# Performance work log

Hardware: AMD Instinct MI355X
Metric: run time of the kernel (lower is better)

Reference implementation:

```python
import jax, jax.numpy as jnp
import numpy as np

B, H, S, D, R = 2, 32, 1024, 128, 16
NB = 4  # max blocks: pre-image, image, pre-assistant-end, post-assistant


def _make_block_mask():
    # Synthetic but realistic block boundaries per sample (derived from the
    # image-token run and assistant-token subsequence positions that the torch
    # module extracts host-side from input_ids).
    bounds = [
        [(0, 16), (16, 272), (272, 603), (603, S)],
        [(0, 8), (8, 264), (264, 501), (501, S)],
    ]
    m = np.zeros((B, NB, S), np.float32)
    for b, blocks in enumerate(bounds):
        for n, (s, e) in enumerate(blocks):
            m[b, n, s:e] = 1.0
    return jnp.asarray(m)


def setup_inputs() -> dict:
    key = jax.random.key(0)
    ks = jax.random.split(key, 7)
    hid = H * D  # 4096
    lo = H * R   # 512
    causal_masked = ~jnp.tril(jnp.ones((S, S), bool))  # True = masked
    return {
        "query_states": jax.random.normal(ks[0], (B, H, S, D), jnp.float32),
        "key_states": jax.random.normal(ks[1], (B, H, S, D), jnp.float32),
        "Wqa": jax.random.normal(ks[2], (lo, hid), jnp.float32) / np.sqrt(hid),
        "Wqb": jax.random.normal(ks[3], (hid, lo), jnp.float32) / np.sqrt(lo),
        "Wka": jax.random.normal(ks[4], (lo, hid), jnp.float32) / np.sqrt(hid),
        "Wkb": jax.random.normal(ks[5], (hid, lo), jnp.float32) / np.sqrt(lo),
        "alpha": jax.random.normal(ks[6], (1,), jnp.float32) * 0.01,  # alpha_std
        "block_mask": _make_block_mask(),  # [B, NB, K] 1.0 inside block
        "attention_mask": jnp.broadcast_to(causal_masked, (B, 1, S, S)),
    }


def reference(query_states, key_states, Wqa, Wqb, Wka, Wkb, alpha, block_mask, attention_mask):
    Bb, Hh, Q, Dd = query_states.shape
    scaling = Dd ** -0.5

    # low-rank Q projection: [B,H,Q,D] -> [B,Q,H*D] -> rank -> back
    q = query_states.transpose(0, 2, 1, 3).reshape(Bb, Q, Hh * Dd)
    q = (q @ Wqa.T) @ Wqb.T
    q = q.reshape(Bb, Q, Hh, Dd).transpose(0, 2, 1, 3)

    Kk = key_states.shape[2]
    k = key_states.transpose(0, 2, 1, 3).reshape(Bb, Kk, Hh * Dd)
    k = (k @ Wka.T) @ Wkb.T
    k = k.reshape(Bb, Kk, Hh, Dd).transpose(0, 2, 1, 3)

    scores = jnp.einsum('bhqd,bhkd->bhqk', q, k) * scaling  # [B,H,Q,K]
    neg = jnp.finfo(scores.dtype).min
    scores = jnp.where(attention_mask, neg, scores)
    attn = jax.nn.softmax(scores, axis=-1)

    # block-wise mean pooling with causal-valid counts (mean_pool path)
    valid = (~attention_mask[:, 0]).astype(attn.dtype)       # [B,Q,K]
    masked_attn = attn * valid[:, None]                      # zero masked keys
    counts = jnp.einsum('bqk,bnk->bqn', valid, block_mask)   # [B,Q,NB]
    sums = jnp.einsum('bhqk,bnk->bhqn', masked_attn, block_mask)
    block_scores = sums / jnp.maximum(counts, 1.0)[:, None]  # [B,H,Q,NB]

    # expand block scores back to full [B,H,Q,K] and zero masked positions
    reweight = jnp.einsum('bhqn,bnk->bhqk', block_scores, block_mask)
    reweight = reweight * valid[:, None]
    return alpha[0] * reweight
```

## Files before the change

### kernel.cpp

```cpp
#include <hip/hip_runtime.h>
#include <hip/hip_bf16.h>

typedef float    f32x4 __attribute__((ext_vector_type(4)));
typedef _Float16 f16x8 __attribute__((ext_vector_type(8)));
typedef unsigned int u32;

#define S_LEN 1024
#define NHEAD 32
#define DHEAD 128
#define HID   4096
#define LORA  512
#define MROWS 2048

__device__ __forceinline__ void gload16(const void* g, const void* l) {
  __builtin_amdgcn_global_load_lds(
      (const __attribute__((address_space(1))) u32*)g,
      (__attribute__((address_space(3))) u32*)l, 16, 0, 0);
}

#define XCH  1048576
#define WCH  262144
#define TOTCH (2*XCH + 4*WCH)

__global__ __launch_bounds__(256) void convert_kernel(
    const float* __restrict__ Xq, const float* __restrict__ Xk,
    const float* __restrict__ Wqa, const float* __restrict__ Wka,
    const float* __restrict__ Wqb, const float* __restrict__ Wkb,
    _Float16* __restrict__ XqH, _Float16* __restrict__ XkH,
    _Float16* __restrict__ WaqH, _Float16* __restrict__ WakH,
    _Float16* __restrict__ WbqH, _Float16* __restrict__ WbkH)
{
  for (int c = blockIdx.x * 256 + threadIdx.x; c < TOTCH; c += 2048 * 256) {
    const float* src;
    _Float16* dst;
    if (c < 2 * XCH) {
      const int cc = (c < XCH) ? c : c - XCH;
      const float* X = (c < XCH) ? Xq : Xk;
      _Float16*  XH = (c < XCH) ? XqH : XkH;
      const int row = cc >> 9;
      const int col8 = cc & 511;
      const int h = col8 >> 4, d0 = (col8 & 15) * 8;
      const int b = row >> 10, s = row & 1023;
      src = X + (((size_t)(b * NHEAD + h)) * S_LEN + s) * DHEAD + d0;
      dst = XH + (size_t)row * HID + col8 * 8;
    } else {
      const int cw = c - 2 * XCH;
      const int seg = cw / WCH;
      const int off = (cw - seg * WCH) * 8;
      const float* Ws[4] = {Wqa, Wka, Wqb, Wkb};
      _Float16*  Wd[4] = {WaqH, WakH, WbqH, WbkH};
      src = Ws[seg] + off;
      dst = Wd[seg] + off;
    }
    f32x4 v0 = *(const f32x4*)(src + 0);
    f32x4 v1 = *(const f32x4*)(src + 4);
    f16x8 h8;
#pragma unroll
    for (int i = 0; i < 4; ++i) { h8[i] = (_Float16)v0[i]; h8[i + 4] = (_Float16)v1[i]; }
    *(f16x8*)dst = h8;
  }
}

__global__ __launch_bounds__(256) void gemm1_kernel(
    const _Float16* __restrict__ XqH, const _Float16* __restrict__ WaqH,
    const _Float16* __restrict__ XkH, const _Float16* __restrict__ WakH,
    float* __restrict__ Up)
{
  const int side = blockIdx.z >> 2, ks = blockIdx.z & 3;
  const _Float16* A = side ? XkH : XqH;
  const _Float16* B = side ? WakH : WaqH;
  float* U = Up + ((size_t)(side * 4 + ks)) * (MROWS * LORA);

  __shared__ _Float16 As[2][128 * 32];
  __shared__ _Float16 Bs[2][128 * 32];

  const int t = threadIdx.x, lane = t & 63, w = t >> 6;
  const int wr = w >> 1, wc = w & 1;
  const int m0 = blockIdx.x * 128, n0 = blockIdx.y * 128;
  const int kbeg = ks * 1024;

  const int o0 = w * 1024 + lane * 16;
  const int o1 = o0 + 4096;
  const int r0 = o0 >> 6, k0e = (o0 & 63) >> 1;
  const int r1 = o1 >> 6, k1e = (o1 & 63) >> 1;

  f32x4 acc[4][4] = {};

  {
    char* AsB = (char*)As[0]; char* BsB = (char*)Bs[0];
    gload16(A + (size_t)(m0 + r0) * HID + kbeg + k0e, AsB + w * 1024);
    gload16(A + (size_t)(m0 + r1) * HID + kbeg + k1e, AsB + 4096 + w * 1024);
    gload16(B + (size_t)(n0 + r0) * HID + kbeg + k0e, BsB + w * 1024);
    gload16(B + (size_t)(n0 + r1) * HID + kbeg + k1e, BsB + 4096 + w * 1024);
  }
  __syncthreads();

  for (int step = 0; step < 32; ++step) {
    const int cur = step & 1;
    if (step + 1 < 32) {
      const int kt = kbeg + (step + 1) * 32;
      char* AsB = (char*)As[cur ^ 1]; char* BsB = (char*)Bs[cur ^ 1];
      gload16(A + (size_t)(m0 + r0) * HID + kt + k0e, AsB + w * 1024);
      gload16(A + (size_t)(m0 + r1) * HID + kt + k1e, AsB + 4096 + w * 1024);
      gload16(B + (size_t)(n0 + r0) * HID + kt + k0e, BsB + w * 1024);
      gload16(B + (size_t)(n0 + r1) * HID + kt + k1e, BsB + 4096 + w * 1024);
    }
    const char* AsB = (const char*)As[cur];
    const char* BsB = (const char*)Bs[cur];
    f16x8 af[4], bf[4];
#pragma unroll
    for (int im = 0; im < 4; ++im)
      af[im] = *(const f16x8*)(AsB + (wr * 64 + im * 16 + (lane & 15)) * 64 + (lane >> 4) * 16);
#pragma unroll
    for (int in = 0; in < 4; ++in)
      bf[in] = *(const f16x8*)(BsB + (wc * 64 + in * 16 + (lane & 15)) * 64 + (lane >> 4) * 16);
#pragma unroll
    for (int im = 0; im < 4; ++im)
#pragma unroll
      for (int in = 0; in < 4; ++in)
        acc[im][in] = __builtin_amdgcn_mfma_f32_16x16x32_f16(af[im], bf[in], acc[im][in], 0, 0, 0);
    __syncthreads();
  }

#pragma unroll
  for (int im = 0; im < 4; ++im)
#pragma unroll
    for (int in = 0; in < 4; ++in)
#pragma unroll
      for (int j = 0; j < 4; ++j) {
        const int m = m0 + wr * 64 + im * 16 + (lane >> 4) * 4 + j;
        const int n = n0 + wc * 64 + in * 16 + (lane & 15);
        U[(size_t)m * LORA + n] = acc[im][in][j];
      }
}

__global__ __launch_bounds__(256) void reduce_u(
    const float* __restrict__ Up, _Float16* __restrict__ Uq, _Float16* __restrict__ Uk)
{
  const int idx = blockIdx.x * 256 + threadIdx.x;
  const int side = idx >> 17;
  const int cc = idx & 131071;
  const float* base = Up + (size_t)side * 4 * (MROWS * LORA) + (size_t)cc * 8;
  f32x4 s0 = {0.f,0.f,0.f,0.f}, s1 = {0.f,0.f,0.f,0.f};
#pragma unroll
  for (int p = 0; p < 4; ++p) {
    const float* pp = base + (size_t)p * (MROWS * LORA);
    f32x4 a0 = *(const f32x4*)(pp);
    f32x4 a1 = *(const f32x4*)(pp + 4);
    s0 += a0; s1 += a1;
  }
  f16x8 h;
#pragma unroll
  for (int i = 0; i < 4; ++i) { h[i] = (_Float16)s0[i]; h[i + 4] = (_Float16)s1[i]; }
  _Float16* U = side ? Uk : Uq;
  *(f16x8*)(U + (size_t)cc * 8) = h;
}

__global__ __launch_bounds__(256) void gemm2_kernel(
    const _Float16* __restrict__ Uq, const _Float16* __restrict__ WbqH,
    const _Float16* __restrict__ Uk, const _Float16* __restrict__ WbkH,
    _Float16* __restrict__ Pq, _Float16* __restrict__ Pk)
{
  const _Float16* A = blockIdx.z ? Uk : Uq;
  const _Float16* B = blockIdx.z ? WbkH : WbqH;
  _Float16*       P = blockIdx.z ? Pk : Pq;

  __shared__ _Float16 As[2][128 * 32];
  __shared__ _Float16 Bs[2][128 * 32];

  const int t = threadIdx.x, lane = t & 63, w = t >> 6;
  const int wr = w >> 1, wc = w & 1;
  const int m0 = blockIdx.x * 128, n0 = blockIdx.y * 128;

  const int o0 = w * 1024 + lane * 16;
  const int o1 = o0 + 4096;
  const int r0 = o0 >> 6, k0e = (o0 & 63) >> 1;
  const int r1 = o1 >> 6, k1e = (o1 & 63) >> 1;

  f32x4 acc[4][4] = {};

  {
    char* AsB = (char*)As[0]; char* BsB = (char*)Bs[0];
    gload16(A + (size_t)(m0 + r0) * LORA + k0e, AsB + w * 1024);
    gload16(A + (size_t)(m0 + r1) * LORA + k1e, AsB + 4096 + w * 1024);
    gload16(B + (size_t)(n0 + r0) * LORA + k0e, BsB + w * 1024);
    gload16(B + (size_t)(n0 + r1) * LORA + k1e, BsB + 4096 + w * 1024);
  }
  __syncthreads();

  for (int step = 0; step < 16; ++step) {
    const int cur = step & 1;
    if (step + 1 < 16) {
      const int kt = (step + 1) * 32;
      char* AsB = (char*)As[cur ^ 1]; char* BsB = (char*)Bs[cur ^ 1];
      gload16(A + (size_t)(m0 + r0) * LORA + kt + k0e, AsB + w * 1024);
      gload16(A + (size_t)(m0 + r1) * LORA + kt + k1e, AsB + 4096 + w * 1024);
      gload16(B + (size_t)(n0 + r0) * LORA + kt + k0e, BsB + w * 1024);
      gload16(B + (size_t)(n0 + r1) * LORA + kt + k1e, BsB + 4096 + w * 1024);
    }
    const char* AsB = (const char*)As[cur];
    const char* BsB = (const char*)Bs[cur];
    f16x8 af[4], bf[4];
#pragma unroll
    for (int im = 0; im < 4; ++im)
      af[im] = *(const f16x8*)(AsB + (wr * 64 + im * 16 + (lane & 15)) * 64 + (lane >> 4) * 16);
#pragma unroll
    for (int in = 0; in < 4; ++in)
      bf[in] = *(const f16x8*)(BsB + (wc * 64 + in * 16 + (lane & 15)) * 64 + (lane >> 4) * 16);
#pragma unroll
    for (int im = 0; im < 4; ++im)
#pragma unroll
      for (int in = 0; in < 4; ++in)
        acc[im][in] = __builtin_amdgcn_mfma_f32_16x16x32_f16(af[im], bf[in], acc[im][in], 0, 0, 0);
    __syncthreads();
  }

#pragma unroll
  for (int im = 0; im < 4; ++im)
#pragma unroll
    for (int in = 0; in < 4; ++in)
#pragma unroll
      for (int j = 0; j < 4; ++j) {
        const int m = m0 + wr * 64 + im * 16 + (lane >> 4) * 4 + j;
        const int n = n0 + wc * 64 + in * 16 + (lane & 15);
        P[(size_t)m * HID + n] = (_Float16)acc[im][in][j];
      }
}

__global__ __launch_bounds__(256) void attn_kernel(
    const _Float16* __restrict__ QP, const _Float16* __restrict__ KP,
    const float* __restrict__ bmask, const float* __restrict__ alphap,
    float* __restrict__ out)
{
  __shared__ float    bm[1024 * 4];
  __shared__ float    pf[1024 * 4];
  __shared__ _Float16 kv[64 * 136];
  __shared__ float    bs_l[64 * 4];

  const int t = threadIdx.x;
  const int lane = t & 63, w = t >> 6;
  const int bh = blockIdx.x, b = bh >> 5, h = bh & 31;
  const int qb = (int)(gridDim.y - 1) - (int)blockIdx.y;

  for (int idx = t; idx < 4096; idx += 256) {
    const int nb = idx >> 10, k = idx & 1023;
    bm[k * 4 + nb] = bmask[(size_t)b * 4096 + idx];
  }
  __syncthreads();

  {
    float carry = 0.f;
    for (int seg = 0; seg < 16; ++seg) {
      float v = bm[(seg * 64 + lane) * 4 + w];
#pragma unroll
      for (int d = 1; d < 64; d <<= 1) {
        float u = __shfl_up(v, d, 64);
        if (lane >= d) v += u;
      }
      pf[(seg * 64 + lane) * 4 + w] = v + carry;
      carry += __shfl(v, 63, 64);
    }
  }

  const int qrow = qb * 64 + w * 16 + (lane & 15);
  const _Float16* qrp = QP + (size_t)(b * 1024 + qrow) * HID + h * DHEAD;
  f16x8 a[4];
#pragma unroll
  for (int i = 0; i < 4; ++i)
    a[i] = *(const f16x8*)(qrp + i * 32 + (lane >> 4) * 8);

  float bsum[4][4] = {};
  const float scale = 0.08838834764831845f;

  const int r = t >> 2, c = (t & 3) * 32;
  const _Float16* kbase = KP + (size_t)(b * 1024) * HID + h * DHEAD;

  for (int kt = 0; kt <= qb; ++kt) {
    const _Float16* pk = kbase + (size_t)(kt * 64 + r) * HID + c;
    f16x8 k0 = *(const f16x8*)(pk + 0);
    f16x8 k1 = *(const f16x8*)(pk + 8);
    f16x8 k2 = *(const f16x8*)(pk + 16);
    f16x8 k3 = *(const f16x8*)(pk + 24);
    __syncthreads();
    *(f16x8*)&kv[r * 136 + c + 0]  = k0;
    *(f16x8*)&kv[r * 136 + c + 8]  = k1;
    *(f16x8*)&kv[r * 136 + c + 16] = k2;
    *(f16x8*)&kv[r * 136 + c + 24] = k3;
    __syncthreads();

    const bool last = (kt == qb);
#pragma unroll
    for (int nt = 0; nt < 4; ++nt) {
      if (last && nt > w) break;
      f32x4 sacc = {0.f, 0.f, 0.f, 0.f};
#pragma unroll
      for (int i = 0; i < 4; ++i) {
        f16x8 bf = *(const f16x8*)&kv[(nt * 16 + (lane & 15)) * 136 + i * 32 + (lane >> 4) * 8];
        sacc = __builtin_amdgcn_mfma_f32_16x16x32_f16(a[i], bf, sacc, 0, 0, 0);
      }
      const int kk = kt * 64 + nt * 16 + (lane & 15);
      f32x4 mv = *(const f32x4*)&bm[kk * 4];
      const bool diag = last && (nt == w);
#pragma unroll
      for (int j = 0; j < 4; ++j) {
        float e = __expf(sacc[j] * scale);
        if (diag) {
          const int q = qb * 64 + w * 16 + (lane >> 4) * 4 + j;
          e = (kk <= q) ? e : 0.f;
        }
        bsum[0][j] += e * mv[0];
        bsum[1][j] += e * mv[1];
        bsum[2][j] += e * mv[2];
        bsum[3][j] += e * mv[3];
      }
    }
  }

#pragma unroll
  for (int j = 0; j < 4; ++j)
#pragma unroll
    for (int m = 1; m < 16; m <<= 1)
#pragma unroll
      for (int nb = 0; nb < 4; ++nb)
        bsum[nb][j] += __shfl_xor(bsum[nb][j], m, 64);

  const float alpha = alphap[0];
  if ((lane & 15) == 0) {
#pragma unroll
    for (int j = 0; j < 4; ++j) {
      const int rr = w * 16 + (lane >> 4) * 4 + j;
      const int q = qb * 64 + rr;
      const float Lr = bsum[0][j] + bsum[1][j] + bsum[2][j] + bsum[3][j];
      const float ainvL = alpha / Lr;
#pragma unroll
      for (int nb = 0; nb < 4; ++nb)
        bs_l[rr * 4 + nb] = bsum[nb][j] * ainvL / fmaxf(pf[q * 4 + nb], 1.f);
    }
  }
  __syncthreads();

  const size_t obase = ((size_t)bh * 1024 + (size_t)qb * 64) * 1024;
  const int k0 = t * 4;
  f32x4 m0v = *(const f32x4*)&bm[(k0 + 0) * 4];
  f32x4 m1v = *(const f32x4*)&bm[(k0 + 1) * 4];
  f32x4 m2v = *(const f32x4*)&bm[(k0 + 2) * 4];
  f32x4 m3v = *(const f32x4*)&bm[(k0 + 3) * 4];
  for (int rr = 0; rr < 64; ++rr) {
    const int q = qb * 64 + rr;
    f32x4 bsv = *(const f32x4*)&bs_l[rr * 4];
    f32x4 o;
    o[0] = (k0 + 0 <= q) ? (bsv[0]*m0v[0] + bsv[1]*m0v[1] + bsv[2]*m0v[2] + bsv[3]*m0v[3]) : 0.f;
    o[1] = (k0 + 1 <= q) ? (bsv[0]*m1v[0] + bsv[1]*m1v[1] + bsv[2]*m1v[2] + bsv[3]*m1v[3]) : 0.f;
    o[2] = (k0 + 2 <= q) ? (bsv[0]*m2v[0] + bsv[1]*m2v[1] + bsv[2]*m2v[2] + bsv[3]*m2v[3]) : 0.f;
    o[3] = (k0 + 3 <= q) ? (bsv[0]*m3v[0] + bsv[1]*m3v[1] + bsv[2]*m3v[2] + bsv[3]*m3v[3]) : 0.f;
    *(f32x4*)(out + obase + (size_t)rr * 1024 + k0) = o;
  }
}

extern "C" void kernel_launch(void* const* d_in, const int* in_sizes, int n_in,
                              void* d_out, int out_size, void* d_ws, size_t ws_size,
                              hipStream_t stream) {
  const float* q     = (const float*)d_in[0];
  const float* k     = (const float*)d_in[1];
  const float* Wqa   = (const float*)d_in[2];
  const float* Wqb   = (const float*)d_in[3];
  const float* Wka   = (const float*)d_in[4];
  const float* Wkb   = (const float*)d_in[5];
  const float* alpha = (const float*)d_in[6];
  const float* bmask = (const float*)d_in[7];
  float* out = (float*)d_out;

  _Float16* XqH  = (_Float16*)d_ws;
  _Float16* XkH  = XqH  + (size_t)MROWS * HID;
  _Float16* WaqH = XkH  + (size_t)MROWS * HID;
  _Float16* WakH = WaqH + (size_t)LORA * HID;
  _Float16* WbqH = WakH + (size_t)LORA * HID;
  _Float16* WbkH = WbqH + (size_t)HID * LORA;
  _Float16* Uq   = WbkH + (size_t)HID * LORA;
  _Float16* Uk   = Uq   + (size_t)MROWS * LORA;
  _Float16* Pq   = Uk   + (size_t)MROWS * LORA;
  _Float16* Pk   = Pq   + (size_t)MROWS * HID;
  float*    Up   = (float*)(Pk + (size_t)MROWS * HID);

  convert_kernel<<<2048, 256, 0, stream>>>(q, k, Wqa, Wka, Wqb, Wkb,
                                           XqH, XkH, WaqH, WakH, WbqH, WbkH);
  gemm1_kernel<<<dim3(16, 4, 8), 256, 0, stream>>>(XqH, WaqH, XkH, WakH, Up);
  reduce_u    <<<1024, 256, 0, stream>>>(Up, Uq, Uk);
  gemm2_kernel<<<dim3(16, 32, 2), 256, 0, stream>>>(Uq, WbqH, Uk, WbkH, Pq, Pk);
  attn_kernel <<<dim3(64, 16), 256, 0, stream>>>(Pq, Pk, bmask, alpha, out);
}
```

Baseline: 457.8 us.

## Fuse fp32-to-fp16 conversion into GEMM loads and prefetch K tiles in attention

```diff
diff --git a/kernel.cpp b/kernel.cpp
--- a/kernel.cpp
+++ b/kernel.cpp
@@ -18,57 +18,23 @@
       (__attribute__((address_space(3))) u32*)l, 16, 0, 0);
 }
 
-#define XCH  1048576
-#define WCH  262144
-#define TOTCH (2*XCH + 4*WCH)
-
-__global__ __launch_bounds__(256) void convert_kernel(
-    const float* __restrict__ Xq, const float* __restrict__ Xk,
-    const float* __restrict__ Wqa, const float* __restrict__ Wka,
-    const float* __restrict__ Wqb, const float* __restrict__ Wkb,
-    _Float16* __restrict__ XqH, _Float16* __restrict__ XkH,
-    _Float16* __restrict__ WaqH, _Float16* __restrict__ WakH,
-    _Float16* __restrict__ WbqH, _Float16* __restrict__ WbkH)
-{
-  for (int c = blockIdx.x * 256 + threadIdx.x; c < TOTCH; c += 2048 * 256) {
-    const float* src;
-    _Float16* dst;
-    if (c < 2 * XCH) {
-      const int cc = (c < XCH) ? c : c - XCH;
-      const float* X = (c < XCH) ? Xq : Xk;
-      _Float16*  XH = (c < XCH) ? XqH : XkH;
-      const int row = cc >> 9;
-      const int col8 = cc & 511;
-      const int h = col8 >> 4, d0 = (col8 & 15) * 8;
-      const int b = row >> 10, s = row & 1023;
-      src = X + (((size_t)(b * NHEAD + h)) * S_LEN + s) * DHEAD + d0;
-      dst = XH + (size_t)row * HID + col8 * 8;
-    } else {
-      const int cw = c - 2 * XCH;
-      const int seg = cw / WCH;
-      const int off = (cw - seg * WCH) * 8;
-      const float* Ws[4] = {Wqa, Wka, Wqb, Wkb};
-      _Float16*  Wd[4] = {WaqH, WakH, WbqH, WbkH};
-      src = Ws[seg] + off;
-      dst = Wd[seg] + off;
-    }
-    f32x4 v0 = *(const f32x4*)(src + 0);
-    f32x4 v1 = *(const f32x4*)(src + 4);
-    f16x8 h8;
-#pragma unroll
-    for (int i = 0; i < 4; ++i) { h8[i] = (_Float16)v0[i]; h8[i + 4] = (_Float16)v1[i]; }
-    *(f16x8*)dst = h8;
-  }
+__device__ __forceinline__ f16x8 cvt8(f32x4 a, f32x4 b) {
+  f16x8 r;
+  r[0] = (_Float16)a[0]; r[1] = (_Float16)a[1];
+  r[2] = (_Float16)a[2]; r[3] = (_Float16)a[3];
+  r[4] = (_Float16)b[0]; r[5] = (_Float16)b[1];
+  r[6] = (_Float16)b[2]; r[7] = (_Float16)b[3];
+  return r;
 }
 
 __global__ __launch_bounds__(256) void gemm1_kernel(
-    const _Float16* __restrict__ XqH, const _Float16* __restrict__ WaqH,
-    const _Float16* __restrict__ XkH, const _Float16* __restrict__ WakH,
+    const float* __restrict__ Xq, const float* __restrict__ Wqa_,
+    const float* __restrict__ Xk, const float* __restrict__ Wka_,
     float* __restrict__ Up)
 {
   const int side = blockIdx.z >> 2, ks = blockIdx.z & 3;
-  const _Float16* A = side ? XkH : XqH;
-  const _Float16* B = side ? WakH : WaqH;
+  const float* X = side ? Xk : Xq;
+  const float* W = side ? Wka_ : Wqa_;
   float* U = Up + ((size_t)(side * 4 + ks)) * (MROWS * LORA);
 
   __shared__ _Float16 As[2][128 * 32];
@@ -79,47 +45,47 @@
   const int m0 = blockIdx.x * 128, n0 = blockIdx.y * 128;
   const int kbeg = ks * 1024;
 
-  const int o0 = w * 1024 + lane * 16;
-  const int o1 = o0 + 4096;
-  const int r0 = o0 >> 6, k0e = (o0 & 63) >> 1;
-  const int r1 = o1 >> 6, k1e = (o1 & 63) >> 1;
-
+  const int ar = t >> 1, ac = (t & 1) * 16;
+  const int am = m0 + ar, ab = am >> 10, as_ = am & 1023;
+  const float* Abase = X + (size_t)ab * (NHEAD * S_LEN * DHEAD) + (size_t)as_ * DHEAD;
+  const float* Brow = W + (size_t)(n0 + ar) * HID;
+
+  f16x8 ha0, ha1, hb0, hb1;
+  auto LOADREGS = [&](int kt) {
+    const int kg = kt + ac;
+    const float* pa = Abase + (size_t)(kg >> 7) * (S_LEN * DHEAD) + (kg & 127);
+    f32x4 a0 = *(const f32x4*)(pa + 0), a1 = *(const f32x4*)(pa + 4);
+    f32x4 a2 = *(const f32x4*)(pa + 8), a3 = *(const f32x4*)(pa + 12);
+    const float* pb = Brow + kg;
+    f32x4 b0 = *(const f32x4*)(pb + 0), b1 = *(const f32x4*)(pb + 4);
+    f32x4 b2 = *(const f32x4*)(pb + 8), b3 = *(const f32x4*)(pb + 12);
+    ha0 = cvt8(a0, a1); ha1 = cvt8(a2, a3);
+    hb0 = cvt8(b0, b1); hb1 = cvt8(b2, b3);
+  };
+
+  LOADREGS(kbeg);
   f32x4 acc[4][4] = {};
-
-  {
-    char* AsB = (char*)As[0]; char* BsB = (char*)Bs[0];
-    gload16(A + (size_t)(m0 + r0) * HID + kbeg + k0e, AsB + w * 1024);
-    gload16(A + (size_t)(m0 + r1) * HID + kbeg + k1e, AsB + 4096 + w * 1024);
-    gload16(B + (size_t)(n0 + r0) * HID + kbeg + k0e, BsB + w * 1024);
-    gload16(B + (size_t)(n0 + r1) * HID + kbeg + k1e, BsB + 4096 + w * 1024);
-  }
-  __syncthreads();
 
   for (int step = 0; step < 32; ++step) {
     const int cur = step & 1;
-    if (step + 1 < 32) {
-      const int kt = kbeg + (step + 1) * 32;
-      char* AsB = (char*)As[cur ^ 1]; char* BsB = (char*)Bs[cur ^ 1];
-      gload16(A + (size_t)(m0 + r0) * HID + kt + k0e, AsB + w * 1024);
-      gload16(A + (size_t)(m0 + r1) * HID + kt + k1e, AsB + 4096 + w * 1024);
-      gload16(B + (size_t)(n0 + r0) * HID + kt + k0e, BsB + w * 1024);
-      gload16(B + (size_t)(n0 + r1) * HID + kt + k1e, BsB + 4096 + w * 1024);
-    }
-    const char* AsB = (const char*)As[cur];
-    const char* BsB = (const char*)Bs[cur];
+    *(f16x8*)&As[cur][ar * 32 + ac]     = ha0;
+    *(f16x8*)&As[cur][ar * 32 + ac + 8] = ha1;
+    *(f16x8*)&Bs[cur][ar * 32 + ac]     = hb0;
+    *(f16x8*)&Bs[cur][ar * 32 + ac + 8] = hb1;
+    __syncthreads();
+    if (step + 1 < 32) LOADREGS(kbeg + (step + 1) * 32);
     f16x8 af[4], bf[4];
 #pragma unroll
     for (int im = 0; im < 4; ++im)
-      af[im] = *(const f16x8*)(AsB + (wr * 64 + im * 16 + (lane & 15)) * 64 + (lane >> 4) * 16);
+      af[im] = *(const f16x8*)&As[cur][(wr * 64 + im * 16 + (lane & 15)) * 32 + (lane >> 4) * 8];
 #pragma unroll
     for (int in = 0; in < 4; ++in)
-      bf[in] = *(const f16x8*)(BsB + (wc * 64 + in * 16 + (lane & 15)) * 64 + (lane >> 4) * 16);
+      bf[in] = *(const f16x8*)&Bs[cur][(wc * 64 + in * 16 + (lane & 15)) * 32 + (lane >> 4) * 8];
 #pragma unroll
     for (int im = 0; im < 4; ++im)
 #pragma unroll
       for (int in = 0; in < 4; ++in)
         acc[im][in] = __builtin_amdgcn_mfma_f32_16x16x32_f16(af[im], bf[in], acc[im][in], 0, 0, 0);
-    __syncthreads();
   }
 
 #pragma unroll
@@ -145,9 +111,8 @@
 #pragma unroll
   for (int p = 0; p < 4; ++p) {
     const float* pp = base + (size_t)p * (MROWS * LORA);
-    f32x4 a0 = *(const f32x4*)(pp);
-    f32x4 a1 = *(const f32x4*)(pp + 4);
-    s0 += a0; s1 += a1;
+    s0 += *(const f32x4*)(pp);
+    s1 += *(const f32x4*)(pp + 4);
   }
   f16x8 h;
 #pragma unroll
@@ -157,12 +122,12 @@
 }
 
 __global__ __launch_bounds__(256) void gemm2_kernel(
-    const _Float16* __restrict__ Uq, const _Float16* __restrict__ WbqH,
-    const _Float16* __restrict__ Uk, const _Float16* __restrict__ WbkH,
+    const _Float16* __restrict__ Uq, const float* __restrict__ Wqb_,
+    const _Float16* __restrict__ Uk, const float* __restrict__ Wkb_,
     _Float16* __restrict__ Pq, _Float16* __restrict__ Pk)
 {
   const _Float16* A = blockIdx.z ? Uk : Uq;
-  const _Float16* B = blockIdx.z ? WbkH : WbqH;
+  const float*   Wf = blockIdx.z ? Wkb_ : Wqb_;
   _Float16*       P = blockIdx.z ? Pk : Pq;
 
   __shared__ _Float16 As[2][128 * 32];
@@ -177,42 +142,44 @@
   const int r0 = o0 >> 6, k0e = (o0 & 63) >> 1;
   const int r1 = o1 >> 6, k1e = (o1 & 63) >> 1;
 
+  const int ar = t >> 1, ac = (t & 1) * 16;
+  const float* Brow = Wf + (size_t)(n0 + ar) * LORA;
+
+  auto GLOADA = [&](int buf, int kt) {
+    char* AsB = (char*)As[buf];
+    gload16(A + (size_t)(m0 + r0) * LORA + kt + k0e, AsB + w * 1024);
+    gload16(A + (size_t)(m0 + r1) * LORA + kt + k1e, AsB + 4096 + w * 1024);
+  };
+  f16x8 hb0, hb1;
+  auto LOADB = [&](int kt) {
+    const float* pb = Brow + kt + ac;
+    f32x4 b0 = *(const f32x4*)(pb + 0), b1 = *(const f32x4*)(pb + 4);
+    f32x4 b2 = *(const f32x4*)(pb + 8), b3 = *(const f32x4*)(pb + 12);
+    hb0 = cvt8(b0, b1); hb1 = cvt8(b2, b3);
+  };
+
+  LOADB(0);
+  GLOADA(0, 0);
   f32x4 acc[4][4] = {};
-
-  {
-    char* AsB = (char*)As[0]; char* BsB = (char*)Bs[0];
-    gload16(A + (size_t)(m0 + r0) * LORA + k0e, AsB + w * 1024);
-    gload16(A + (size_t)(m0 + r1) * LORA + k1e, AsB + 4096 + w * 1024);
-    gload16(B + (size_t)(n0 + r0) * LORA + k0e, BsB + w * 1024);
-    gload16(B + (size_t)(n0 + r1) * LORA + k1e, BsB + 4096 + w * 1024);
-  }
-  __syncthreads();
 
   for (int step = 0; step < 16; ++step) {
     const int cur = step & 1;
-    if (step + 1 < 16) {
-      const int kt = (step + 1) * 32;
-      char* AsB = (char*)As[cur ^ 1]; char* BsB = (char*)Bs[cur ^ 1];
-      gload16(A + (size_t)(m0 + r0) * LORA + kt + k0e, AsB + w * 1024);
-      gload16(A + (size_t)(m0 + r1) * LORA + kt + k1e, AsB + 4096 + w * 1024);
-      gload16(B + (size_t)(n0 + r0) * LORA + kt + k0e, BsB + w * 1024);
-      gload16(B + (size_t)(n0 + r1) * LORA + kt + k1e, BsB + 4096 + w * 1024);
-    }
-    const char* AsB = (const char*)As[cur];
-    const char* BsB = (const char*)Bs[cur];
+    *(f16x8*)&Bs[cur][ar * 32 + ac]     = hb0;
+    *(f16x8*)&Bs[cur][ar * 32 + ac + 8] = hb1;
+    __syncthreads();
+    if (step + 1 < 16) { LOADB((step + 1) * 32); GLOADA(cur ^ 1, (step + 1) * 32); }
     f16x8 af[4], bf[4];
 #pragma unroll
     for (int im = 0; im < 4; ++im)
-      af[im] = *(const f16x8*)(AsB + (wr * 64 + im * 16 + (lane & 15)) * 64 + (lane >> 4) * 16);
+      af[im] = *(const f16x8*)&As[cur][(wr * 64 + im * 16 + (lane & 15)) * 32 + (lane >> 4) * 8];
 #pragma unroll
     for (int in = 0; in < 4; ++in)
-      bf[in] = *(const f16x8*)(BsB + (wc * 64 + in * 16 + (lane & 15)) * 64 + (lane >> 4) * 16);
+      bf[in] = *(const f16x8*)&Bs[cur][(wc * 64 + in * 16 + (lane & 15)) * 32 + (lane >> 4) * 8];
 #pragma unroll
     for (int im = 0; im < 4; ++im)
 #pragma unroll
       for (int in = 0; in < 4; ++in)
         acc[im][in] = __builtin_amdgcn_mfma_f32_16x16x32_f16(af[im], bf[in], acc[im][in], 0, 0, 0);
-    __syncthreads();
   }
 
 #pragma unroll
@@ -233,8 +200,8 @@
     float* __restrict__ out)
 {
   __shared__ float    bm[1024 * 4];
-  __shared__ float    pf[1024 * 4];
-  __shared__ _Float16 kv[64 * 136];
+  __shared__ _Float16 kv[2][64 * 136];
+  __shared__ float    pfq[64 * 4];
   __shared__ float    bs_l[64 * 4];
 
   const int t = threadIdx.x;
@@ -250,14 +217,14 @@
 
   {
     float carry = 0.f;
-    for (int seg = 0; seg < 16; ++seg) {
+    for (int seg = 0; seg <= qb; ++seg) {
       float v = bm[(seg * 64 + lane) * 4 + w];
 #pragma unroll
       for (int d = 1; d < 64; d <<= 1) {
         float u = __shfl_up(v, d, 64);
         if (lane >= d) v += u;
       }
-      pf[(seg * 64 + lane) * 4 + w] = v + carry;
+      if (seg == qb) pfq[lane * 4 + w] = v + carry;
       carry += __shfl(v, 63, 64);
     }
   }
@@ -275,18 +242,24 @@
   const int r = t >> 2, c = (t & 3) * 32;
   const _Float16* kbase = KP + (size_t)(b * 1024) * HID + h * DHEAD;
 
+  f16x8 k0, k1, k2, k3;
+  auto LOADK = [&](int kt) {
+    const _Float16* pk = kbase + (size_t)(kt * 64 + r) * HID + c;
+    k0 = *(const f16x8*)(pk + 0);
+    k1 = *(const f16x8*)(pk + 8);
+    k2 = *(const f16x8*)(pk + 16);
+    k3 = *(const f16x8*)(pk + 24);
+  };
+  LOADK(0);
+
   for (int kt = 0; kt <= qb; ++kt) {
-    const _Float16* pk = kbase + (size_t)(kt * 64 + r) * HID + c;
-    f16x8 k0 = *(const f16x8*)(pk + 0);
-    f16x8 k1 = *(const f16x8*)(pk + 8);
-    f16x8 k2 = *(const f16x8*)(pk + 16);
-    f16x8 k3 = *(const f16x8*)(pk + 24);
+    const int cur = kt & 1;
+    *(f16x8*)&kv[cur][r * 136 + c + 0]  = k0;
+    *(f16x8*)&kv[cur][r * 136 + c + 8]  = k1;
+    *(f16x8*)&kv[cur][r * 136 + c + 16] = k2;
+    *(f16x8*)&kv[cur][r * 136 + c + 24] = k3;
     __syncthreads();
-    *(f16x8*)&kv[r * 136 + c + 0]  = k0;
-    *(f16x8*)&kv[r * 136 + c + 8]  = k1;
-    *(f16x8*)&kv[r * 136 + c + 16] = k2;
-    *(f16x8*)&kv[r * 136 + c + 24] = k3;
-    __syncthreads();
+    if (kt < qb) LOADK(kt + 1);
 
     const bool last = (kt == qb);
 #pragma unroll
@@ -295,7 +268,7 @@
       f32x4 sacc = {0.f, 0.f, 0.f, 0.f};
 #pragma unroll
       for (int i = 0; i < 4; ++i) {
-        f16x8 bf = *(const f16x8*)&kv[(nt * 16 + (lane & 15)) * 136 + i * 32 + (lane >> 4) * 8];
+        f16x8 bf = *(const f16x8*)&kv[cur][(nt * 16 + (lane & 15)) * 136 + i * 32 + (lane >> 4) * 8];
         sacc = __builtin_amdgcn_mfma_f32_16x16x32_f16(a[i], bf, sacc, 0, 0, 0);
       }
       const int kk = kt * 64 + nt * 16 + (lane & 15);
@@ -329,31 +302,30 @@
 #pragma unroll
     for (int j = 0; j < 4; ++j) {
       const int rr = w * 16 + (lane >> 4) * 4 + j;
-      const int q = qb * 64 + rr;
       const float Lr = bsum[0][j] + bsum[1][j] + bsum[2][j] + bsum[3][j];
       const float ainvL = alpha / Lr;
 #pragma unroll
       for (int nb = 0; nb < 4; ++nb)
-        bs_l[rr * 4 + nb] = bsum[nb][j] * ainvL / fmaxf(pf[q * 4 + nb], 1.f);
+        bs_l[rr * 4 + nb] = bsum[nb][j] * ainvL / fmaxf(pfq[rr * 4 + nb], 1.f);
     }
   }
   __syncthreads();
 
   const size_t obase = ((size_t)bh * 1024 + (size_t)qb * 64) * 1024;
-  const int k0 = t * 4;
-  f32x4 m0v = *(const f32x4*)&bm[(k0 + 0) * 4];
-  f32x4 m1v = *(const f32x4*)&bm[(k0 + 1) * 4];
-  f32x4 m2v = *(const f32x4*)&bm[(k0 + 2) * 4];
-  f32x4 m3v = *(const f32x4*)&bm[(k0 + 3) * 4];
+  const int k0i = t * 4;
+  f32x4 m0v = *(const f32x4*)&bm[(k0i + 0) * 4];
+  f32x4 m1v = *(const f32x4*)&bm[(k0i + 1) * 4];
+  f32x4 m2v = *(const f32x4*)&bm[(k0i + 2) * 4];
+  f32x4 m3v = *(const f32x4*)&bm[(k0i + 3) * 4];
   for (int rr = 0; rr < 64; ++rr) {
     const int q = qb * 64 + rr;
     f32x4 bsv = *(const f32x4*)&bs_l[rr * 4];
     f32x4 o;
-    o[0] = (k0 + 0 <= q) ? (bsv[0]*m0v[0] + bsv[1]*m0v[1] + bsv[2]*m0v[2] + bsv[3]*m0v[3]) : 0.f;
-    o[1] = (k0 + 1 <= q) ? (bsv[0]*m1v[0] + bsv[1]*m1v[1] + bsv[2]*m1v[2] + bsv[3]*m1v[3]) : 0.f;
-    o[2] = (k0 + 2 <= q) ? (bsv[0]*m2v[0] + bsv[1]*m2v[1] + bsv[2]*m2v[2] + bsv[3]*m2v[3]) : 0.f;
-    o[3] = (k0 + 3 <= q) ? (bsv[0]*m3v[0] + bsv[1]*m3v[1] + bsv[2]*m3v[2] + bsv[3]*m3v[3]) : 0.f;
-    *(f32x4*)(out + obase + (size_t)rr * 1024 + k0) = o;
+    o[0] = (k0i + 0 <= q) ? (bsv[0]*m0v[0] + bsv[1]*m0v[1] + bsv[2]*m0v[2] + bsv[3]*m0v[3]) : 0.f;
+    o[1] = (k0i + 1 <= q) ? (bsv[0]*m1v[0] + bsv[1]*m1v[1] + bsv[2]*m1v[2] + bsv[3]*m1v[3]) : 0.f;
+    o[2] = (k0i + 2 <= q) ? (bsv[0]*m2v[0] + bsv[1]*m2v[1] + bsv[2]*m2v[2] + bsv[3]*m2v[3]) : 0.f;
+    o[3] = (k0i + 3 <= q) ? (bsv[0]*m3v[0] + bsv[1]*m3v[1] + bsv[2]*m3v[2] + bsv[3]*m3v[3]) : 0.f;
+    *(f32x4*)(out + obase + (size_t)rr * 1024 + k0i) = o;
   }
 }
 
@@ -370,22 +342,14 @@
   const float* bmask = (const float*)d_in[7];
   float* out = (float*)d_out;
 
-  _Float16* XqH  = (_Float16*)d_ws;
-  _Float16* XkH  = XqH  + (size_t)MROWS * HID;
-  _Float16* WaqH = XkH  + (size_t)MROWS * HID;
-  _Float16* WakH = WaqH + (size_t)LORA * HID;
-  _Float16* WbqH = WakH + (size_t)LORA * HID;
-  _Float16* WbkH = WbqH + (size_t)HID * LORA;
-  _Float16* Uq   = WbkH + (size_t)HID * LORA;
-  _Float16* Uk   = Uq   + (size_t)MROWS * LORA;
-  _Float16* Pq   = Uk   + (size_t)MROWS * LORA;
-  _Float16* Pk   = Pq   + (size_t)MROWS * HID;
-  float*    Up   = (float*)(Pk + (size_t)MROWS * HID);
-
-  convert_kernel<<<2048, 256, 0, stream>>>(q, k, Wqa, Wka, Wqb, Wkb,
-                                           XqH, XkH, WaqH, WakH, WbqH, WbkH);
-  gemm1_kernel<<<dim3(16, 4, 8), 256, 0, stream>>>(XqH, WaqH, XkH, WakH, Up);
+  _Float16* Uq = (_Float16*)d_ws;
+  _Float16* Uk = Uq + (size_t)MROWS * LORA;
+  _Float16* Pq = Uk + (size_t)MROWS * LORA;
+  _Float16* Pk = Pq + (size_t)MROWS * HID;
+  float*    Up = (float*)(Pk + (size_t)MROWS * HID);
+
+  gemm1_kernel<<<dim3(16, 4, 8), 256, 0, stream>>>(q, Wqa, k, Wka, Up);
   reduce_u    <<<1024, 256, 0, stream>>>(Up, Uq, Uk);
-  gemm2_kernel<<<dim3(16, 32, 2), 256, 0, stream>>>(Uq, WbqH, Uk, WbkH, Pq, Pk);
+  gemm2_kernel<<<dim3(16, 32, 2), 256, 0, stream>>>(Uq, Wqb, Uk, Wkb, Pq, Pk);
   attn_kernel <<<dim3(64, 16), 256, 0, stream>>>(Pq, Pk, bmask, alpha, out);
 }
```

After: 466.6 us. About the same (+1.9%).
